# Optimization experiments

Hardware: AMD Instinct MI355X
Metric: run time of the kernel (lower is better)

Reference implementation:

```python
import jax, jax.numpy as jnp
import numpy as np

V = 50257  # output_size (vocab)
H = 1024   # hidden_size


def setup_inputs() -> dict:
    key = jax.random.key(0)
    ks = jax.random.split(key, 10)
    s = 1.0 / np.sqrt(H)
    return {
        "x": jax.random.randint(ks[0], (1,), 0, V),
        "hidden": jax.random.normal(ks[1], (1, 1, H), dtype=jnp.float32),
        "cell_state": jax.random.normal(ks[2], (1, 1, H), dtype=jnp.float32),
        # learned parameters
        "emb": jax.random.normal(ks[3], (V, H), dtype=jnp.float32),
        "w_ih": jax.random.uniform(ks[4], (4 * H, H), jnp.float32, -s, s),
        "w_hh": jax.random.uniform(ks[5], (4 * H, H), jnp.float32, -s, s),
        "b_ih": jax.random.uniform(ks[6], (4 * H,), jnp.float32, -s, s),
        "b_hh": jax.random.uniform(ks[7], (4 * H,), jnp.float32, -s, s),
        "fc_w": jax.random.uniform(ks[8], (V, H), jnp.float32, -s, s),
        "fc_b": jax.random.uniform(ks[9], (V,), jnp.float32, -s, s),
    }


def reference(x, hidden, cell_state, emb, w_ih, w_hh, b_ih, b_hh, fc_w, fc_b):
    # embedding lookup: [1, H]
    e = emb[x]
    h = hidden[0]      # [1, H]
    c = cell_state[0]  # [1, H]
    # single LSTM step, PyTorch gate order (i, f, g, o)
    gates = e @ w_ih.T + b_ih + h @ w_hh.T + b_hh  # [1, 4H]
    i, f, g, o = jnp.split(gates, 4, axis=-1)
    i = jax.nn.sigmoid(i)
    f = jax.nn.sigmoid(f)
    g = jnp.tanh(g)
    o = jax.nn.sigmoid(o)
    c_new = f * c + i * g
    h_new = o * jnp.tanh(c_new)
    # fc + log-softmax over vocab: [1, V]
    logp = jax.nn.log_softmax(h_new @ fc_w.T + fc_b, axis=1)
    return logp, h_new[None], c_new[None]
```

## Files before the change

### kernel.cpp

```cpp
#include <hip/hip_runtime.h>
#include <hip/hip_bf16.h>
#include <math.h>

#define V 50257
#define H 1024
#define NB_FC 2048
#define NWAVES (NB_FC * 4)
#define NPAIRS ((V + 1) / 2)
#define FC_ITERS ((NPAIRS + NWAVES - 1) / NWAVES)

typedef float vfloat4 __attribute__((ext_vector_type(4)));

__device__ __forceinline__ vfloat4 ntload4(const float* p) {
    return __builtin_nontemporal_load((const vfloat4*)p);
}

__global__ __launch_bounds__(512) void lstm_kernel(
    const int* __restrict__ x,
    const float* __restrict__ hidden,
    const float* __restrict__ cell,
    const float* __restrict__ emb,
    const float* __restrict__ w_ih,
    const float* __restrict__ w_hh,
    const float* __restrict__ b_ih,
    const float* __restrict__ b_hh,
    float* __restrict__ out)
{
    const int k = blockIdx.x;
    const int t = threadIdx.x;
    const int wave = t >> 6;
    const int lane = t & 63;
    const int gate = wave & 3;

    const float* e = emb + (size_t)x[0] * H;
    const float* vec = (wave < 4) ? e : hidden;
    const float* row = ((wave < 4) ? w_ih : w_hh) + (size_t)(gate * H + k) * H;

    float acc = 0.0f;
#pragma unroll
    for (int it = 0; it < 4; ++it) {
        const int off = (it * 64 + lane) * 4;
        const vfloat4 w = ntload4(row + off);
        const float4  v = *(const float4*)(vec + off);
        acc += w.x * v.x + w.y * v.y + w.z * v.z + w.w * v.w;
    }
#pragma unroll
    for (int off = 1; off < 64; off <<= 1)
        acc += __shfl_xor(acc, off, 64);

    __shared__ float g8[8];
    if (lane == 0) g8[wave] = acc;
    __syncthreads();

    if (t == 0) {
        const float gi = g8[0] + g8[4] + b_ih[k]         + b_hh[k];
        const float gf = g8[1] + g8[5] + b_ih[H + k]     + b_hh[H + k];
        const float gg = g8[2] + g8[6] + b_ih[2 * H + k] + b_hh[2 * H + k];
        const float go = g8[3] + g8[7] + b_ih[3 * H + k] + b_hh[3 * H + k];

        const float i_g = 1.0f / (1.0f + expf(-gi));
        const float f_g = 1.0f / (1.0f + expf(-gf));
        const float g_g = tanhf(gg);
        const float o_g = 1.0f / (1.0f + expf(-go));

        const float c_new = f_g * cell[k] + i_g * g_g;
        const float h_new = o_g * tanhf(c_new);

        out[V + k]     = h_new;
        out[V + H + k] = c_new;
    }
}

__global__ __launch_bounds__(256, 8) void fc_kernel(
    const float* __restrict__ fc_w,
    const float* __restrict__ fc_b,
    const float* __restrict__ h_new,
    float* __restrict__ logits,
    float* __restrict__ partials)
{
    const int t = threadIdx.x;
    const int wave = t >> 6;
    const int lane = t & 63;
    const int wid = blockIdx.x * 4 + wave;

    float4 hv[4];
#pragma unroll
    for (int it = 0; it < 4; ++it)
        hv[it] = *(const float4*)(h_new + (it * 64 + lane) * 4);

    float s = 0.0f;

#pragma unroll
    for (int j = 0; j < FC_ITERS; ++j) {
        const int p = j * NWAVES + wid;
        if (p < NPAIRS) {
            const int v0 = p * 2;
            const bool has1 = (v0 + 1 < V);
            const float* r0 = fc_w + (size_t)v0 * H;
            const float* r1 = r0 + (has1 ? H : 0);

            float a0 = 0.0f, a1 = 0.0f;
#pragma unroll
            for (int it = 0; it < 4; ++it) {
                const int off = (it * 64 + lane) * 4;
                const vfloat4 w0 = ntload4(r0 + off);
                const vfloat4 w1 = ntload4(r1 + off);
                a0 += w0.x * hv[it].x + w0.y * hv[it].y + w0.z * hv[it].z + w0.w * hv[it].w;
                a1 += w1.x * hv[it].x + w1.y * hv[it].y + w1.z * hv[it].z + w1.w * hv[it].w;
            }
#pragma unroll
            for (int off = 1; off < 64; off <<= 1) {
                a0 += __shfl_xor(a0, off, 64);
                a1 += __shfl_xor(a1, off, 64);
            }
            a0 += fc_b[v0];
            if (lane == 0) logits[v0] = a0;
            s += __expf(a0);
            if (has1) {
                a1 += fc_b[v0 + 1];
                if (lane == 0) logits[v0 + 1] = a1;
                s += __expf(a1);
            }
        }
    }

    __shared__ float ws4[4];
    if (lane == 0) ws4[wave] = s;
    __syncthreads();
    if (t == 0)
        partials[blockIdx.x] = ws4[0] + ws4[1] + ws4[2] + ws4[3];
}

__global__ __launch_bounds__(256) void logp_kernel(
    const float* __restrict__ logits,
    const float* __restrict__ partials,
    float* __restrict__ out)
{
    const int t = threadIdx.x;
    const int lane = t & 63;
    const int wave = t >> 6;

    float s = 0.0f;
#pragma unroll
    for (int i = 0; i < 2; ++i) {
        const float4 p = *(const float4*)(partials + (t * 2 + i) * 4);
        s += p.x + p.y + p.z + p.w;
    }
#pragma unroll
    for (int off = 1; off < 64; off <<= 1)
        s += __shfl_xor(s, off, 64);

    __shared__ float red[4];
    __shared__ float sub_s;
    if (lane == 0) red[wave] = s;
    __syncthreads();
    if (t == 0)
        sub_s = logf(red[0] + red[1] + red[2] + red[3]);
    __syncthreads();
    const float sub = sub_s;

    const int base = (blockIdx.x * 256 + t) * 4;
    if (base + 3 < V) {
        const float4 l = *(const float4*)(logits + base);
        float4 o;
        o.x = l.x - sub; o.y = l.y - sub; o.z = l.z - sub; o.w = l.w - sub;
        *(float4*)(out + base) = o;
    } else {
#pragma unroll
        for (int j = 0; j < 4; ++j) {
            const int v = base + j;
            if (v < V) out[v] = logits[v] - sub;
        }
    }
}

extern "C" void kernel_launch(void* const* d_in, const int* in_sizes, int n_in,
                              void* d_out, int out_size, void* d_ws, size_t ws_size,
                              hipStream_t stream)
{
    const int*   x      = (const int*)  d_in[0];
    const float* hidden = (const float*)d_in[1];
    const float* cell   = (const float*)d_in[2];
    const float* emb    = (const float*)d_in[3];
    const float* w_ih   = (const float*)d_in[4];
    const float* w_hh   = (const float*)d_in[5];
    const float* b_ih   = (const float*)d_in[6];
    const float* b_hh   = (const float*)d_in[7];
    const float* fc_w   = (const float*)d_in[8];
    const float* fc_b   = (const float*)d_in[9];
    float* out = (float*)d_out;

    float* logits   = (float*)d_ws;
    float* partials = (float*)((char*)d_ws + 201088);

    lstm_kernel<<<H, 512, 0, stream>>>(x, hidden, cell, emb, w_ih, w_hh,
                                       b_ih, b_hh, out);
    fc_kernel<<<NB_FC, 256, 0, stream>>>(fc_w, fc_b, out + V, logits, partials);
    logp_kernel<<<(V + 1023) / 1024, 256, 0, stream>>>(logits, partials, out);
}
```

Before: 45.41 us.

## Fuse LSTM step and FC into one persistent kernel with atomic grid barrier

Merges the LSTM gate kernel and the FC kernel into a single launch of 1536 blocks. The first 1024 blocks compute the LSTM step and bump an atomic counter, and every block prefetches its first FC weight row before spin-waiting on that counter. This aims to hide one launch gap and overlap FC weight loading with the LSTM computation. In exchange it adds a memset launch and an intra-grid spin barrier, which can deadlock if not all blocks are co-resident, and the grid gets fewer FC waves.

```diff
diff --git a/kernel.cpp b/kernel.cpp
--- a/kernel.cpp
+++ b/kernel.cpp
@@ -4,10 +4,11 @@
 
 #define V 50257
 #define H 1024
-#define NB_FC 2048
-#define NWAVES (NB_FC * 4)
+#define NB 1536
+#define NWAVES (NB * 4)
 #define NPAIRS ((V + 1) / 2)
 #define FC_ITERS ((NPAIRS + NWAVES - 1) / NWAVES)
+#define NPROD 1024
 
 typedef float vfloat4 __attribute__((ext_vector_type(4)));
 
@@ -15,7 +16,7 @@
     return __builtin_nontemporal_load((const vfloat4*)p);
 }
 
-__global__ __launch_bounds__(512) void lstm_kernel(
+__global__ __launch_bounds__(256, 6) void fused_kernel(
     const int* __restrict__ x,
     const float* __restrict__ hidden,
     const float* __restrict__ cell,
@@ -24,65 +25,82 @@
     const float* __restrict__ w_hh,
     const float* __restrict__ b_ih,
     const float* __restrict__ b_hh,
-    float* __restrict__ out)
+    const float* __restrict__ fc_w,
+    const float* __restrict__ fc_b,
+    float* __restrict__ out,
+    float* __restrict__ logits,
+    float* __restrict__ partials,
+    int* __restrict__ done)
 {
-    const int k = blockIdx.x;
+    const int b = blockIdx.x;
     const int t = threadIdx.x;
     const int wave = t >> 6;
     const int lane = t & 63;
-    const int gate = wave & 3;
-
-    const float* e = emb + (size_t)x[0] * H;
-    const float* vec = (wave < 4) ? e : hidden;
-    const float* row = ((wave < 4) ? w_ih : w_hh) + (size_t)(gate * H + k) * H;
-
-    float acc = 0.0f;
-#pragma unroll
-    for (int it = 0; it < 4; ++it) {
-        const int off = (it * 64 + lane) * 4;
-        const vfloat4 w = ntload4(row + off);
-        const float4  v = *(const float4*)(vec + off);
-        acc += w.x * v.x + w.y * v.y + w.z * v.z + w.w * v.w;
-    }
-#pragma unroll
-    for (int off = 1; off < 64; off <<= 1)
-        acc += __shfl_xor(acc, off, 64);
-
-    __shared__ float g8[8];
-    if (lane == 0) g8[wave] = acc;
-    __syncthreads();
+
+    __shared__ float g4[4];
+    __shared__ float ws4[4];
+
+    if (b < NPROD) {
+        const float* e = emb + (size_t)x[0] * H;
+        const float* rih = w_ih + (size_t)(wave * H + b) * H;
+        const float* rhh = w_hh + (size_t)(wave * H + b) * H;
+
+        float acc = 0.0f;
+#pragma unroll
+        for (int it = 0; it < 4; ++it) {
+            const int off = (it * 64 + lane) * 4;
+            const vfloat4 wi = ntload4(rih + off);
+            const vfloat4 wh = ntload4(rhh + off);
+            const float4  ev = *(const float4*)(e + off);
+            const float4  hv = *(const float4*)(hidden + off);
+            acc += wi.x * ev.x + wi.y * ev.y + wi.z * ev.z + wi.w * ev.w;
+            acc += wh.x * hv.x + wh.y * hv.y + wh.z * hv.z + wh.w * hv.w;
+        }
+#pragma unroll
+        for (int off = 1; off < 64; off <<= 1)
+            acc += __shfl_xor(acc, off, 64);
+
+        if (lane == 0) g4[wave] = acc;
+        __syncthreads();
+
+        if (t == 0) {
+            const float gi = g4[0] + b_ih[b]         + b_hh[b];
+            const float gf = g4[1] + b_ih[H + b]     + b_hh[H + b];
+            const float gg = g4[2] + b_ih[2 * H + b] + b_hh[2 * H + b];
+            const float go = g4[3] + b_ih[3 * H + b] + b_hh[3 * H + b];
+
+            const float i_g = 1.0f / (1.0f + expf(-gi));
+            const float f_g = 1.0f / (1.0f + expf(-gf));
+            const float g_g = tanhf(gg);
+            const float o_g = 1.0f / (1.0f + expf(-go));
+
+            const float c_new = f_g * cell[b] + i_g * g_g;
+            const float h_new = o_g * tanhf(c_new);
+
+            out[V + b]     = h_new;
+            out[V + H + b] = c_new;
+            __hip_atomic_fetch_add(done, 1, __ATOMIC_RELEASE,
+                                   __HIP_MEMORY_SCOPE_AGENT);
+        }
+    }
+
+    const int wid = b * 4 + wave;
+    const float* pre_row = fc_w + (size_t)(wid * 2) * H;
+    vfloat4 pw[4];
+#pragma unroll
+    for (int it = 0; it < 4; ++it)
+        pw[it] = ntload4(pre_row + (it * 64 + lane) * 4);
 
     if (t == 0) {
-        const float gi = g8[0] + g8[4] + b_ih[k]         + b_hh[k];
-        const float gf = g8[1] + g8[5] + b_ih[H + k]     + b_hh[H + k];
-        const float gg = g8[2] + g8[6] + b_ih[2 * H + k] + b_hh[2 * H + k];
-        const float go = g8[3] + g8[7] + b_ih[3 * H + k] + b_hh[3 * H + k];
-
-        const float i_g = 1.0f / (1.0f + expf(-gi));
-        const float f_g = 1.0f / (1.0f + expf(-gf));
-        const float g_g = tanhf(gg);
-        const float o_g = 1.0f / (1.0f + expf(-go));
-
-        const float c_new = f_g * cell[k] + i_g * g_g;
-        const float h_new = o_g * tanhf(c_new);
-
-        out[V + k]     = h_new;
-        out[V + H + k] = c_new;
-    }
-}
-
-__global__ __launch_bounds__(256, 8) void fc_kernel(
-    const float* __restrict__ fc_w,
-    const float* __restrict__ fc_b,
-    const float* __restrict__ h_new,
-    float* __restrict__ logits,
-    float* __restrict__ partials)
-{
-    const int t = threadIdx.x;
-    const int wave = t >> 6;
-    const int lane = t & 63;
-    const int wid = blockIdx.x * 4 + wave;
-
+        while (__hip_atomic_load(done, __ATOMIC_RELAXED,
+                                 __HIP_MEMORY_SCOPE_AGENT) < NPROD)
+            __builtin_amdgcn_s_sleep(8);
+        (void)__hip_atomic_load(done, __ATOMIC_ACQUIRE,
+                                __HIP_MEMORY_SCOPE_AGENT);
+    }
+    __syncthreads();
+
+    const float* __restrict__ h_new = out + V;
     float4 hv[4];
 #pragma unroll
     for (int it = 0; it < 4; ++it)
@@ -93,7 +111,7 @@
 #pragma unroll
     for (int j = 0; j < FC_ITERS; ++j) {
         const int p = j * NWAVES + wid;
-        if (p < NPAIRS) {
+        if (j == 0 || p < NPAIRS) {
             const int v0 = p * 2;
             const bool has1 = (v0 + 1 < V);
             const float* r0 = fc_w + (size_t)v0 * H;
@@ -103,7 +121,7 @@
 #pragma unroll
             for (int it = 0; it < 4; ++it) {
                 const int off = (it * 64 + lane) * 4;
-                const vfloat4 w0 = ntload4(r0 + off);
+                const vfloat4 w0 = (j == 0) ? pw[it] : ntload4(r0 + off);
                 const vfloat4 w1 = ntload4(r1 + off);
                 a0 += w0.x * hv[it].x + w0.y * hv[it].y + w0.z * hv[it].z + w0.w * hv[it].w;
                 a1 += w1.x * hv[it].x + w1.y * hv[it].y + w1.z * hv[it].z + w1.w * hv[it].w;
@@ -124,11 +142,10 @@
         }
     }
 
-    __shared__ float ws4[4];
     if (lane == 0) ws4[wave] = s;
     __syncthreads();
     if (t == 0)
-        partials[blockIdx.x] = ws4[0] + ws4[1] + ws4[2] + ws4[3];
+        partials[b] = ws4[0] + ws4[1] + ws4[2] + ws4[3];
 }
 
 __global__ __launch_bounds__(256) void logp_kernel(
@@ -142,10 +159,8 @@
 
     float s = 0.0f;
 #pragma unroll
-    for (int i = 0; i < 2; ++i) {
-        const float4 p = *(const float4*)(partials + (t * 2 + i) * 4);
-        s += p.x + p.y + p.z + p.w;
-    }
+    for (int i = 0; i < 6; ++i)
+        s += partials[t * 6 + i];
 #pragma unroll
     for (int off = 1; off < 64; off <<= 1)
         s += __shfl_xor(s, off, 64);
@@ -192,9 +207,11 @@
 
     float* logits   = (float*)d_ws;
     float* partials = (float*)((char*)d_ws + 201088);
-
-    lstm_kernel<<<H, 512, 0, stream>>>(x, hidden, cell, emb, w_ih, w_hh,
-                                       b_ih, b_hh, out);
-    fc_kernel<<<NB_FC, 256, 0, stream>>>(fc_w, fc_b, out + V, logits, partials);
+    int*   done     = (int*)((char*)d_ws + 208000);
+
+    hipMemsetAsync(done, 0, sizeof(int), stream);
+    fused_kernel<<<NB, 256, 0, stream>>>(x, hidden, cell, emb, w_ih, w_hh,
+                                         b_ih, b_hh, fc_w, fc_b, out,
+                                         logits, partials, done);
     logp_kernel<<<(V + 1023) / 1024, 256, 0, stream>>>(logits, partials, out);
 }
```

New measurement: 155.9 us. 243% more time.
